# Optimization experiments

Measured on AMD Instinct MI355X. Metric: run time of the kernel, lower is better.

## Reference

```python
import jax, jax.numpy as jnp
import numpy as np

C, W = 144, 77          # channel_count, batch_width
KW = 10                 # kernel_width
FC = 64                 # fc_segment_length
CONV_OUT = W - KW + 1   # 68
H2 = 128

def setup_inputs() -> dict:
    key = jax.random.key(0)
    ks = jax.random.split(key, 10)
    s_fc = 1.0 / np.sqrt(W)
    s2 = 1.0 / np.sqrt(C * FC + CONV_OUT)
    s3 = 1.0 / np.sqrt(H2)
    s_cv = 1.0 / np.sqrt(C * KW)
    return {
        "x": jax.random.normal(ks[0], (C, W), dtype=jnp.float32),
        "fc_w": jax.random.uniform(ks[1], (C, FC, W), minval=-s_fc, maxval=s_fc, dtype=jnp.float32),
        "fc_b": jax.random.uniform(ks[2], (C, FC), minval=-s_fc, maxval=s_fc, dtype=jnp.float32),
        "conv_w": jax.random.uniform(ks[3], (1, 1, C, KW), minval=-s_cv, maxval=s_cv, dtype=jnp.float32),
        "conv_b": jax.random.uniform(ks[4], (1,), minval=-s_cv, maxval=s_cv, dtype=jnp.float32),
        "w2": jax.random.uniform(ks[5], (H2, C * FC + CONV_OUT), minval=-s2, maxval=s2, dtype=jnp.float32),
        "b2": jax.random.uniform(ks[6], (H2,), minval=-s2, maxval=s2, dtype=jnp.float32),
        "w3": jax.random.uniform(ks[7], (1, H2), minval=-s3, maxval=s3, dtype=jnp.float32),
        "b3": jax.random.uniform(ks[8], (1,), minval=-s3, maxval=s3, dtype=jnp.float32),
    }

def reference(x, fc_w, fc_b, conv_w, conv_b, w2, b2, w3, b3):
    # 144 per-channel Linear(77,64) fused into one batched GEMV: [C,FC,W] @ [C,W] -> [C,FC]
    fc_out = jnp.einsum('cdw,cw->cd', fc_w, x) + fc_b   # [C, FC]
    fc_out = fc_out.reshape(-1)                          # [C*FC]
    # Conv2d(1,1,(C,KW),stride=1) over full-height input -> [CONV_OUT]
    conv = jax.lax.conv_general_dilated(
        x[None, None, :, :], conv_w,
        window_strides=(1, 1), padding='VALID',
        dimension_numbers=('NCHW', 'OIHW', 'NCHW'))     # [1,1,1,CONV_OUT]
    conv = conv.reshape(-1) + conv_b[0]                  # [CONV_OUT]
    concat = jnp.concatenate([fc_out, conv])             # [C*FC + CONV_OUT]
    h = jax.nn.relu(concat @ w2.T + b2)                  # [H2]
    out = jax.nn.relu(h @ w3.T + b3)                     # [1]
    return jax.nn.sigmoid(out)
```

## Files before the change

### kernel.cpp

```cpp
#include <hip/hip_runtime.h>
#include <math.h>

#define CC 144
#define WW 77
#define KW 10
#define FC 64
#define CONV_OUT 68
#define H2 128
#define CONCAT (CC*FC + CONV_OUT)
#define BLOCK 384

__global__ __launch_bounds__(BLOCK, 1) void fused_mlp_kernel(
    const float* __restrict__ x,
    const float* __restrict__ fc_w,
    const float* __restrict__ fc_b,
    const float* __restrict__ conv_w,
    const float* __restrict__ conv_b,
    const float* __restrict__ w2,
    const float* __restrict__ b2,
    const float* __restrict__ w3,
    const float* __restrict__ b3,
    float* __restrict__ out,
    float* __restrict__ h_accum,
    unsigned int* __restrict__ counter)
{
    __shared__ float xs[WW];
    __shared__ float vals[CONV_OUT];
    __shared__ float xfull[CC*WW];
    __shared__ float cw[CC*KW];
    __shared__ float red[BLOCK/64];
    __shared__ unsigned int is_last;

    const int t = threadIdx.x;
    const int blk = blockIdx.x;

    float hpart = 0.0f;

    if (blk < CC) {
        const int c = blk;
        if (t < WW) xs[t] = x[c*WW + t];
        __syncthreads();
        if (t < FC*4) {
            const int d = t >> 2, p = t & 3;
            const float* wrow = fc_w + (size_t)(c*FC + d)*WW;
            float s = 0.f;
            for (int w = p; w < WW; w += 4) s += wrow[w] * xs[w];
            s += __shfl_down(s, 2, 4);
            s += __shfl_down(s, 1, 4);
            if (p == 0) vals[d] = s + fc_b[c*FC + d];
        }
        __syncthreads();
        if (t < H2) {
            const float* wrow = w2 + (size_t)t*CONCAT + c*FC;
            float s = 0.f;
            #pragma unroll
            for (int d = 0; d < FC; ++d) s += wrow[d] * vals[d];
            hpart = s;
        }
    } else {
        for (int i = t; i < CC*WW; i += BLOCK) xfull[i] = x[i];
        for (int i = t; i < CC*KW; i += BLOCK) cw[i] = conv_w[i];
        __syncthreads();
        if (t < CONV_OUT*4) {
            const int j = t >> 2, p = t & 3;
            float s = 0.f;
            for (int c = p; c < CC; c += 4) {
                const float* xr = xfull + c*WW + j;
                const float* wr = cw + c*KW;
                #pragma unroll
                for (int k = 0; k < KW; ++k) s += xr[k] * wr[k];
            }
            s += __shfl_down(s, 2, 4);
            s += __shfl_down(s, 1, 4);
            if (p == 0) vals[j] = s + conv_b[0];
        }
        __syncthreads();
        if (t < H2) {
            const float* wrow = w2 + (size_t)t*CONCAT + CC*FC;
            float s = 0.f;
            #pragma unroll
            for (int j = 0; j < CONV_OUT; ++j) s += wrow[j] * vals[j];
            hpart = s;
        }
    }

    if (t < H2) atomicAdd(&h_accum[t], hpart);
    __threadfence();
    __syncthreads();
    if (t == 0) {
        unsigned int done = atomicAdd(counter, 1u);
        is_last = (done == gridDim.x - 1) ? 1u : 0u;
    }
    __syncthreads();

    if (is_last) {
        float v = 0.f;
        if (t < H2) {
            float hv = atomicAdd(&h_accum[t], 0.0f) + b2[t];
            hv = fmaxf(hv, 0.f);
            v = hv * w3[t];
        }
        #pragma unroll
        for (int off = 32; off > 0; off >>= 1) v += __shfl_down(v, off, 64);
        if ((t & 63) == 0) red[t >> 6] = v;
        __syncthreads();
        if (t == 0) {
            float s = 0.f;
            #pragma unroll
            for (int i = 0; i < BLOCK/64; ++i) s += red[i];
            s = fmaxf(s + b3[0], 0.f);
            out[0] = 1.0f / (1.0f + expf(-s));
        }
    }
}

extern "C" void kernel_launch(void* const* d_in, const int* in_sizes, int n_in,
                              void* d_out, int out_size, void* d_ws, size_t ws_size,
                              hipStream_t stream) {
    const float* x      = (const float*)d_in[0];
    const float* fc_w   = (const float*)d_in[1];
    const float* fc_b   = (const float*)d_in[2];
    const float* conv_w = (const float*)d_in[3];
    const float* conv_b = (const float*)d_in[4];
    const float* w2     = (const float*)d_in[5];
    const float* b2     = (const float*)d_in[6];
    const float* w3     = (const float*)d_in[7];
    const float* b3     = (const float*)d_in[8];
    float* out = (float*)d_out;

    float* h_accum = (float*)d_ws;
    unsigned int* counter = (unsigned int*)((char*)d_ws + H2*sizeof(float));

    hipMemsetAsync(d_ws, 0, (H2 + 1) * sizeof(float), stream);

    fused_mlp_kernel<<<CC + 1, BLOCK, 0, stream>>>(
        x, fc_w, fc_b, conv_w, conv_b, w2, b2, w3, b3,
        out, h_accum, counter);
}
```

Baseline: 101.3 us.

## Split fused kernel into partials and finale kernels, drop atomics and memset

Replaces the atomic accumulation plus last-block-done counter with a two-kernel scheme. Each block writes its per-H2 partial row to workspace, and a single-block finale kernel sums the rows and applies the output layers. This removes the memset launch, the atomics and the threadfence. It also shrinks the block size to 256, which halves the conv work split per output. The cost is one extra kernel launch and a serial 145-row sum in the finale.

```diff
diff --git a/kernel.cpp b/kernel.cpp
--- a/kernel.cpp
+++ b/kernel.cpp
@@ -8,39 +8,30 @@
 #define CONV_OUT 68
 #define H2 128
 #define CONCAT (CC*FC + CONV_OUT)
-#define BLOCK 384
+#define NBLK (CC + 1)
 
-__global__ __launch_bounds__(BLOCK, 1) void fused_mlp_kernel(
+__global__ __launch_bounds__(256, 1) void partials_kernel(
     const float* __restrict__ x,
     const float* __restrict__ fc_w,
     const float* __restrict__ fc_b,
     const float* __restrict__ conv_w,
     const float* __restrict__ conv_b,
     const float* __restrict__ w2,
-    const float* __restrict__ b2,
-    const float* __restrict__ w3,
-    const float* __restrict__ b3,
-    float* __restrict__ out,
-    float* __restrict__ h_accum,
-    unsigned int* __restrict__ counter)
+    float* __restrict__ partial)
 {
     __shared__ float xs[WW];
     __shared__ float vals[CONV_OUT];
     __shared__ float xfull[CC*WW];
     __shared__ float cw[CC*KW];
-    __shared__ float red[BLOCK/64];
-    __shared__ unsigned int is_last;
 
     const int t = threadIdx.x;
     const int blk = blockIdx.x;
-
-    float hpart = 0.0f;
 
     if (blk < CC) {
         const int c = blk;
         if (t < WW) xs[t] = x[c*WW + t];
         __syncthreads();
-        if (t < FC*4) {
+        {
             const int d = t >> 2, p = t & 3;
             const float* wrow = fc_w + (size_t)(c*FC + d)*WW;
             float s = 0.f;
@@ -55,23 +46,22 @@
             float s = 0.f;
             #pragma unroll
             for (int d = 0; d < FC; ++d) s += wrow[d] * vals[d];
-            hpart = s;
+            partial[(size_t)blk*H2 + t] = s;
         }
     } else {
-        for (int i = t; i < CC*WW; i += BLOCK) xfull[i] = x[i];
-        for (int i = t; i < CC*KW; i += BLOCK) cw[i] = conv_w[i];
+        for (int i = t; i < CC*WW; i += 256) xfull[i] = x[i];
+        for (int i = t; i < CC*KW; i += 256) cw[i] = conv_w[i];
         __syncthreads();
-        if (t < CONV_OUT*4) {
-            const int j = t >> 2, p = t & 3;
+        if (t < CONV_OUT*2) {
+            const int j = t >> 1, p = t & 1;
             float s = 0.f;
-            for (int c = p; c < CC; c += 4) {
+            for (int c = p; c < CC; c += 2) {
                 const float* xr = xfull + c*WW + j;
                 const float* wr = cw + c*KW;
                 #pragma unroll
                 for (int k = 0; k < KW; ++k) s += xr[k] * wr[k];
             }
-            s += __shfl_down(s, 2, 4);
-            s += __shfl_down(s, 1, 4);
+            s += __shfl_down(s, 1, 2);
             if (p == 0) vals[j] = s + conv_b[0];
         }
         __syncthreads();
@@ -80,37 +70,34 @@
             float s = 0.f;
             #pragma unroll
             for (int j = 0; j < CONV_OUT; ++j) s += wrow[j] * vals[j];
-            hpart = s;
+            partial[(size_t)blk*H2 + t] = s;
         }
     }
+}
 
-    if (t < H2) atomicAdd(&h_accum[t], hpart);
-    __threadfence();
+__global__ __launch_bounds__(128, 1) void finale_kernel(
+    const float* __restrict__ partial,
+    const float* __restrict__ b2,
+    const float* __restrict__ w3,
+    const float* __restrict__ b3,
+    float* __restrict__ out)
+{
+    __shared__ float red[2];
+    const int t = threadIdx.x;
+
+    float s = b2[t];
+    for (int b = 0; b < NBLK; ++b)
+        s += partial[(size_t)b*H2 + t];
+    s = fmaxf(s, 0.f);
+    float v = s * w3[t];
+
+    #pragma unroll
+    for (int off = 32; off > 0; off >>= 1) v += __shfl_down(v, off, 64);
+    if ((t & 63) == 0) red[t >> 6] = v;
     __syncthreads();
     if (t == 0) {
-        unsigned int done = atomicAdd(counter, 1u);
-        is_last = (done == gridDim.x - 1) ? 1u : 0u;
-    }
-    __syncthreads();
-
-    if (is_last) {
-        float v = 0.f;
-        if (t < H2) {
-            float hv = atomicAdd(&h_accum[t], 0.0f) + b2[t];
-            hv = fmaxf(hv, 0.f);
-            v = hv * w3[t];
-        }
-        #pragma unroll
-        for (int off = 32; off > 0; off >>= 1) v += __shfl_down(v, off, 64);
-        if ((t & 63) == 0) red[t >> 6] = v;
-        __syncthreads();
-        if (t == 0) {
-            float s = 0.f;
-            #pragma unroll
-            for (int i = 0; i < BLOCK/64; ++i) s += red[i];
-            s = fmaxf(s + b3[0], 0.f);
-            out[0] = 1.0f / (1.0f + expf(-s));
-        }
+        float r = fmaxf(red[0] + red[1] + b3[0], 0.f);
+        out[0] = 1.0f / (1.0f + expf(-r));
     }
 }
 
@@ -128,12 +115,9 @@
     const float* b3     = (const float*)d_in[8];
     float* out = (float*)d_out;
 
-    float* h_accum = (float*)d_ws;
-    unsigned int* counter = (unsigned int*)((char*)d_ws + H2*sizeof(float));
+    float* partial = (float*)d_ws;
 
-    hipMemsetAsync(d_ws, 0, (H2 + 1) * sizeof(float), stream);
-
-    fused_mlp_kernel<<<CC + 1, BLOCK, 0, stream>>>(
-        x, fc_w, fc_b, conv_w, conv_b, w2, b2, w3, b3,
-        out, h_accum, counter);
+    partials_kernel<<<NBLK, 256, 0, stream>>>(
+        x, fc_w, fc_b, conv_w, conv_b, w2, partial);
+    finale_kernel<<<1, 128, 0, stream>>>(partial, b2, w3, b3, out);
 }
```

New measurement: 93.82 us. 7.4% less time.
